# Optimization experiments

Hardware: AMD Instinct MI355X
Metric: run time of the kernel (lower is better)

Reference implementation:

```python
import jax, jax.numpy as jnp
import numpy as np

EPS_BN = 1e-5   # torch BatchNorm1d default eps
K = 3           # de_neighbors


def conv1(x, w):
    # 1x1 Conv1d, no bias: x [B,C,N], w [O,C] -> [B,O,N]
    return jnp.einsum('oc,bcn->bon', w, x)


def bn_relu(y, g, b):
    # BatchNorm1d in training mode (batch statistics, biased variance) + ReLU
    mean = jnp.mean(y, axis=(0, 2), keepdims=True)
    var = jnp.var(y, axis=(0, 2), keepdims=True)
    yn = (y - mean) * jax.lax.rsqrt(var + EPS_BN)
    return jax.nn.relu(yn * g[None, :, None] + b[None, :, None])


def propagate(xyz1, xyz2, p1, p2, k):
    # xyz1 [B,N,3] fine coords, xyz2 [B,S,3] coarse coords,
    # p1 [B,D1,N] fine feats, p2 [B,D2,S] coarse feats -> [B,D1+D2,N]
    pts2 = p2.transpose(0, 2, 1)  # [B,S,D2]
    # squared pairwise distances [B,N,S]
    d = (jnp.sum(xyz1 ** 2, -1)[:, :, None]
         + jnp.sum(xyz2 ** 2, -1)[:, None, :]
         - 2.0 * jnp.einsum('bnc,bsc->bns', xyz1, xyz2))
    negd, idx = jax.lax.top_k(-d, k)          # k smallest distances
    dists = -negd                              # [B,N,k]
    w = 1.0 / (dists + 1e-8)
    w = w / jnp.sum(w, -1, keepdims=True)      # inverse-distance weights
    B = xyz1.shape[0]
    gathered = pts2[jnp.arange(B)[:, None, None], idx]     # [B,N,k,D2]
    interp = jnp.sum(gathered * w[..., None], axis=2)      # [B,N,D2]
    new = jnp.concatenate([p1.transpose(0, 2, 1), interp], axis=-1)
    return new.transpose(0, 2, 1)


def setup_inputs() -> dict:
    key = jax.random.key(0)
    ks = jax.random.split(key, 20)
    B = 16
    npts = [2048, 512, 128, 32, 8]
    ch = [64, 128, 256, 512, 1024]
    inp = {}
    for i in range(5):
        inp[f'xyz{i}'] = jax.random.normal(ks[i], (B, npts[i], 3), jnp.float32)
        inp[f'x{i}'] = jax.random.normal(ks[5 + i], (B, ch[i], npts[i]), jnp.float32)
    lin_dims = [1536, 1792, 1920, 1984]
    for i, dmid in enumerate(lin_dims):
        inp[f'w_lin{i}'] = jax.random.normal(ks[10 + i], (dmid, dmid), jnp.float32) * (1.0 / np.sqrt(dmid))
        inp[f'g_lin{i}'] = jnp.ones((dmid,), jnp.float32)
        inp[f'b_lin{i}'] = jnp.zeros((dmid,), jnp.float32)
    inp['w_dec0'] = jax.random.normal(ks[14], (256, 1984), jnp.float32) * (1.0 / np.sqrt(1984))
    inp['g_dec'] = jnp.ones((256,), jnp.float32)
    inp['b_dec'] = jnp.zeros((256,), jnp.float32)
    inp['w_dec1'] = jax.random.normal(ks[15], (1, 256), jnp.float32) * (1.0 / np.sqrt(256))
    return inp


def reference(xyz0, xyz1, xyz2, xyz3, xyz4,
              x0, x1, x2, x3, x4,
              w_lin0, g_lin0, b_lin0,
              w_lin1, g_lin1, b_lin1,
              w_lin2, g_lin2, b_lin2,
              w_lin3, g_lin3, b_lin3,
              w_dec0, g_dec, b_dec, w_dec1):
    # lists are reversed in forward: coarsest first
    x = x4
    x = propagate(xyz3, xyz4, x3, x, K)   # [B,1536,32]
    x = bn_relu(conv1(x, w_lin0), g_lin0, b_lin0)
    x = propagate(xyz2, xyz3, x2, x, K)   # [B,1792,128]
    x = bn_relu(conv1(x, w_lin1), g_lin1, b_lin1)
    x = propagate(xyz1, xyz2, x1, x, K)   # [B,1920,512]
    x = bn_relu(conv1(x, w_lin2), g_lin2, b_lin2)
    x = propagate(xyz0, xyz1, x0, x, K)   # [B,1984,2048]
    x = bn_relu(conv1(x, w_lin3), g_lin3, b_lin3)
    # str_dec: Linear1Layer(1984,256) -> Dropout(eval=identity) -> Conv1d(256,1)
    x = bn_relu(conv1(x, w_dec0), g_dec, b_dec)
    out = conv1(x, w_dec1)                # [B,1,N]
    return out.squeeze(1)                 # [B,N]
```

## Files before the change

kernel.cpp:

```cpp
#include <hip/hip_runtime.h>
#include <stdint.h>
#include <stddef.h>

typedef _Float16 half8 __attribute__((ext_vector_type(8)));
typedef _Float16 half4v __attribute__((ext_vector_type(4)));
typedef float f32x4 __attribute__((ext_vector_type(4)));

__device__ __forceinline__ void gload_lds16(const void* g, void* l) {
  __builtin_amdgcn_global_load_lds((const __attribute__((address_space(1))) void*)g,
                                   (__attribute__((address_space(3))) void*)l, 16, 0, 0);
}

struct TPack {
  const float* in[5];
  _Float16* out[5];
  int C[5], N[5];
  int cum[6];
};
__global__ __launch_bounds__(256) void k_transpose_all(TPack p) {
  __shared__ float tile[32][33];
  int t = blockIdx.x;
  int ti = 0;
#pragma unroll
  for (int i = 0; i < 5; ++i) if (t >= p.cum[i + 1]) ti = i + 1;
  int lt = t - p.cum[ti];
  int C = p.C[ti], N = p.N[ti];
  const float* in = p.in[ti];
  _Float16* out = p.out[ti];
  int tiles_n = (N + 31) / 32;
  int perb = (C / 32) * tiles_n;
  int b = lt / perb;
  int rem = lt - b * perb;
  int c0 = (rem / tiles_n) * 32;
  int n0 = (rem % tiles_n) * 32;
  int tx = threadIdx.x, ty = threadIdx.y;
#pragma unroll
  for (int j = 0; j < 32; j += 8) {
    int c = c0 + ty + j, n = n0 + tx;
    if (c < C && n < N) tile[ty + j][tx] = in[((size_t)b * C + c) * N + n];
  }
  __syncthreads();
#pragma unroll
  for (int j = 0; j < 32; j += 8) {
    int n = n0 + ty + j, c = c0 + tx;
    if (n < N && c < C) out[((size_t)b * N + n) * C + c] = (_Float16)tile[tx][ty + j];
  }
}

__global__ __launch_bounds__(256) void k_cast_pad_w(const float* __restrict__ W,
                                                    _Float16* __restrict__ Wh,
                                                    int O, int K, int Opad, int Kpad) {
  size_t i = ((size_t)blockIdx.x * 256 + threadIdx.x) * 4;
  if (i >= (size_t)Opad * Kpad) return;
  int r = (int)(i / Kpad), k = (int)(i % Kpad);
  half4v v;
#pragma unroll
  for (int j = 0; j < 4; ++j) {
    float f = (r < O && (k + j) < K) ? W[(size_t)r * K + k + j] : 0.f;
    v[j] = (_Float16)f;
  }
  *(half4v*)(Wh + i) = v;
}

struct KPack {
  const float* q[4]; const float* p[4];
  int N1[4], S[4];
  int cum[5];
  int obase[4];
};
#define KNN_INS(dd, ii) { float _d = (dd); int _i = (ii); \
  if (_d < d0)      { d2 = d1; i2 = i1; d1 = d0; i1 = i0; d0 = _d; i0 = _i; } \
  else if (_d < d1) { d2 = d1; i2 = i1; d1 = _d; i1 = _i; } \
  else if (_d < d2) { d2 = _d; i2 = _i; } }
__global__ __launch_bounds__(256) void k_knn_all(KPack kp, int4* __restrict__ idxo,
                                                 float4* __restrict__ wo) {
  __shared__ float sp[512 * 3];
  __shared__ float spp[512];
  int t = blockIdx.x;
  int st = 0;
#pragma unroll
  for (int i = 0; i < 4; ++i) if (t >= kp.cum[i + 1]) st = i + 1;
  int lb = t - kp.cum[st];
  int N1 = kp.N1[st], S = kp.S[st];
  int nb = (N1 * 4 + 255) / 256;
  int b = lb / nb;
  int xb = lb - b * nb;
  const float* p = kp.p[st];
  const float* q = kp.q[st];
  for (int i = threadIdx.x; i < S * 3; i += 256) sp[i] = p[(size_t)b * S * 3 + i];
  __syncthreads();
  for (int s = threadIdx.x; s < S; s += 256)
    spp[s] = sp[s * 3] * sp[s * 3] + sp[s * 3 + 1] * sp[s * 3 + 1] + sp[s * 3 + 2] * sp[s * 3 + 2];
  __syncthreads();
  int tt = xb * 256 + threadIdx.x;
  int n = tt >> 2, sub = tt & 3;
  if (n >= N1) return;
  const float* qp = q + ((size_t)b * N1 + n) * 3;
  float qx = qp[0], qy = qp[1], qz = qp[2];
  float qq = qx * qx + qy * qy + qz * qz;
  float d0 = 1e30f, d1 = 1e30f, d2 = 1e30f;
  int i0 = 0, i1 = 0, i2 = 0;
  int Sq = S >> 2;
  int s0 = sub * Sq;
  for (int i = 0; i < Sq; ++i) {
    int s = s0 + i;
    float d = qq + spp[s] - 2.f * (qx * sp[s * 3] + qy * sp[s * 3 + 1] + qz * sp[s * 3 + 2]);
    KNN_INS(d, s);
  }
#pragma unroll
  for (int m = 1; m <= 2; m <<= 1) {
    float rd0 = __shfl_xor(d0, m, 64), rd1 = __shfl_xor(d1, m, 64), rd2 = __shfl_xor(d2, m, 64);
    int   ri0 = __shfl_xor(i0, m, 64), ri1 = __shfl_xor(i1, m, 64), ri2 = __shfl_xor(i2, m, 64);
    KNN_INS(rd0, ri0); KNN_INS(rd1, ri1); KNN_INS(rd2, ri2);
  }
  if (sub == 0) {
    float w0 = 1.f / (d0 + 1e-8f), w1 = 1.f / (d1 + 1e-8f), w2 = 1.f / (d2 + 1e-8f);
    float wsum = w0 + w1 + w2;
    int gi = kp.obase[st] + b * N1 + n;
    idxo[gi] = make_int4(b * S + i0, b * S + i1, b * S + i2, 0);
    wo[gi] = make_float4(w0 / wsum, w1 / wsum, w2 / wsum, 0.f);
  }
}

__global__ __launch_bounds__(256) void k_bn_norm(_Float16* __restrict__ G,
                                                 const float* __restrict__ scale,
                                                 const float* __restrict__ shiftv,
                                                 size_t total8, int ld) {
  size_t i = (size_t)blockIdx.x * 256 + threadIdx.x;
  if (i >= total8) return;
  half8 v = *(half8*)&G[i * 8];
  int c0 = (int)((i * 8) % (size_t)ld);
#pragma unroll
  for (int j = 0; j < 8; ++j) {
    float f = (float)v[j] * scale[c0 + j] + shiftv[c0 + j];
    v[j] = (_Float16)fmaxf(f, 0.f);
  }
  *(half8*)&G[i * 8] = v;
}

__global__ __launch_bounds__(256) void k_bn_finalize(const float* __restrict__ sum,
                                                     const float* __restrict__ sumsq,
                                                     const float* __restrict__ g, const float* __restrict__ b,
                                                     float* __restrict__ scale, float* __restrict__ shiftv,
                                                     int O, int Opad, float invM) {
  int c = blockIdx.x * 256 + threadIdx.x;
  if (c >= Opad) return;
  if (c < O) {
    float mean = sum[c] * invM;
    float var = sumsq[c] * invM - mean * mean;
    float sc = g[c] * rsqrtf(var + 1e-5f);
    scale[c] = sc;
    shiftv[c] = b[c] - mean * sc;
  } else {
    scale[c] = 0.f;
    shiftv[c] = 0.f;
  }
}


__global__ __launch_bounds__(256) void k_gemm_anorm(const _Float16* __restrict__ A,
                                                    const float* __restrict__ scale,
                                                    const float* __restrict__ shift,
                                                    int apply_nr,
                                                    const _Float16* __restrict__ W,
                                                    _Float16* __restrict__ Cout,
                                                    int K, int lda, int ldb, int ldc) {
  __shared__ __align__(16) _Float16 lA[128 * 64];
  __shared__ __align__(16) _Float16 lB[128 * 64];
  int tid = threadIdx.x;
  int m0 = blockIdx.x * 128;
  int o0 = blockIdx.y * 128;
  int lane = tid & 63, wv = tid >> 6;
  int wm = (wv & 1) * 64, wo = (wv >> 1) * 64;
  int lr = lane & 15, lq = lane >> 4;
  int trow = tid >> 3;
  int tsegl = (((tid & 7) ^ (trow & 7))) * 8;
  int sw = lr & 7;

  f32x4 acc[4][4];
#pragma unroll
  for (int mi = 0; mi < 4; ++mi)
#pragma unroll
    for (int oi = 0; oi < 4; ++oi)
      acc[mi][oi] = (f32x4){0.f, 0.f, 0.f, 0.f};

  const _Float16* gA = A + (size_t)(m0 + trow) * lda + tsegl;
  const _Float16* gB = W + (size_t)(o0 + trow) * ldb + tsegl;

  for (int k0 = 0; k0 < K; k0 += 64) {
#pragma unroll
    for (int i = 0; i < 4; ++i)
      gload_lds16(gB + (size_t)(32 * i) * ldb + k0, lB + ((size_t)i * 256 + tid) * 8);
    if (apply_nr) {
      float sc[8], sh[8];
#pragma unroll
      for (int j = 0; j < 8; ++j) { sc[j] = scale[k0 + tsegl + j]; sh[j] = shift[k0 + tsegl + j]; }
#pragma unroll
      for (int i = 0; i < 4; ++i) {
        half8 v = *(const half8*)(gA + (size_t)(32 * i) * lda + k0);
        half8 o;
#pragma unroll
        for (int j = 0; j < 8; ++j)
          o[j] = (_Float16)fmaxf((float)v[j] * sc[j] + sh[j], 0.f);
        *(half8*)&lA[((size_t)i * 256 + tid) * 8] = o;
      }
    } else {
#pragma unroll
      for (int i = 0; i < 4; ++i)
        gload_lds16(gA + (size_t)(32 * i) * lda + k0, lA + ((size_t)i * 256 + tid) * 8);
    }
    __syncthreads();
#pragma unroll
    for (int ks = 0; ks < 64; ks += 32) {
      half8 af[4], bf[4];
#pragma unroll
      for (int mi = 0; mi < 4; ++mi)
        af[mi] = *(const half8*)&lA[(wm + mi * 16 + lr) * 64 + ((((ks >> 3) + lq) ^ sw)) * 8];
#pragma unroll
      for (int oi = 0; oi < 4; ++oi)
        bf[oi] = *(const half8*)&lB[(wo + oi * 16 + lr) * 64 + ((((ks >> 3) + lq) ^ sw)) * 8];
#pragma unroll
      for (int mi = 0; mi < 4; ++mi)
#pragma unroll
        for (int oi = 0; oi < 4; ++oi)
          acc[mi][oi] = __builtin_amdgcn_mfma_f32_16x16x32_f16(af[mi], bf[oi], acc[mi][oi], 0, 0, 0);
    }
    __syncthreads();
  }

#pragma unroll
  for (int mi = 0; mi < 4; ++mi)
#pragma unroll
    for (int oi = 0; oi < 4; ++oi) {
      int col = o0 + wo + oi * 16 + lr;
      int rowb = m0 + wm + mi * 16 + lq * 4;
#pragma unroll
      for (int r = 0; r < 4; ++r)
        Cout[(size_t)(rowb + r) * ldc + col] = (_Float16)acc[mi][oi][r];
    }
}

__global__ __launch_bounds__(256) void k_gemm_yis(const _Float16* __restrict__ A,
                                                  const _Float16* __restrict__ W,
                                                  const _Float16* __restrict__ Z,
                                                  const int4* __restrict__ idxb,
                                                  const float4* __restrict__ wb,
                                                  _Float16* __restrict__ Y,
                                                  float* __restrict__ sum,
                                                  float* __restrict__ sumsq,
                                                  int K, int lda, int ldb, int ldy,
                                                  int ldz, int zcol0, int swz) {
  __shared__ __align__(16) _Float16 lsm[2 * 128 * 64];
  __shared__ int4 sIdx[128];
  __shared__ float4 sWt[128];
  __shared__ float sStat[256];
  _Float16* lA = lsm;
  _Float16* lB = lsm + 128 * 64;
  int tid = threadIdx.x;
  int m0, o0;
  if (swz) {
    int bid = blockIdx.y * gridDim.x + blockIdx.x;
    int o = (bid & 7) + ((bid >> 11) << 3);
    int m = (bid >> 3) & 255;
    m0 = m * 128; o0 = o * 128;
  } else {
    m0 = blockIdx.x * 128; o0 = blockIdx.y * 128;
  }
  if (tid < 128) {
    sIdx[tid] = idxb[m0 + tid];
    sWt[tid] = wb[m0 + tid];
  }
  sStat[tid] = 0.f;
  int lane = tid & 63, wv = tid >> 6;
  int wm = (wv & 1) * 64, wo = (wv >> 1) * 64;
  int lr = lane & 15, lq = lane >> 4;
  int trow = tid >> 3;
  int tsegl = (((tid & 7) ^ (trow & 7))) * 8;
  int sw = lr & 7;

  f32x4 acc[4][4];
#pragma unroll
  for (int mi = 0; mi < 4; ++mi)
#pragma unroll
    for (int oi = 0; oi < 4; ++oi)
      acc[mi][oi] = (f32x4){0.f, 0.f, 0.f, 0.f};

  const _Float16* gA = A + (size_t)(m0 + trow) * lda + tsegl;
  const _Float16* gB = W + (size_t)(o0 + trow) * ldb + tsegl;

  for (int k0 = 0; k0 < K; k0 += 64) {
#pragma unroll
    for (int i = 0; i < 4; ++i) {
      gload_lds16(gA + (size_t)(32 * i) * lda + k0, lA + ((size_t)i * 256 + tid) * 8);
      gload_lds16(gB + (size_t)(32 * i) * ldb + k0, lB + ((size_t)i * 256 + tid) * 8);
    }
    __syncthreads();
#pragma unroll
    for (int ks = 0; ks < 64; ks += 32) {
      half8 af[4], bf[4];
#pragma unroll
      for (int mi = 0; mi < 4; ++mi)
        af[mi] = *(const half8*)&lA[(wm + mi * 16 + lr) * 64 + ((((ks >> 3) + lq) ^ sw)) * 8];
#pragma unroll
      for (int oi = 0; oi < 4; ++oi)
        bf[oi] = *(const half8*)&lB[(wo + oi * 16 + lr) * 64 + ((((ks >> 3) + lq) ^ sw)) * 8];
#pragma unroll
      for (int mi = 0; mi < 4; ++mi)
#pragma unroll
        for (int oi = 0; oi < 4; ++oi)
          acc[mi][oi] = __builtin_amdgcn_mfma_f32_16x16x32_f16(af[mi], bf[oi], acc[mi][oi], 0, 0, 0);
    }
    __syncthreads();
  }

#pragma unroll
  for (int mi = 0; mi < 4; ++mi)
#pragma unroll
    for (int oi = 0; oi < 4; ++oi)
#pragma unroll
      for (int r = 0; r < 4; ++r)
        lsm[(wm + mi * 16 + lq * 4 + r) * 128 + (wo + oi * 16 + lr)] = (_Float16)acc[mi][oi][r];
  __syncthreads();

  int tcol = (tid & 15) * 8;
  int rbase = tid >> 4;
  float s8[8], q8[8];
#pragma unroll
  for (int j = 0; j < 8; ++j) { s8[j] = 0.f; q8[j] = 0.f; }
#pragma unroll
  for (int i = 0; i < 8; ++i) {
    int row = rbase + i * 16;
    int4 id = sIdx[row];
    float4 w = sWt[row];
    half8 y = *(half8*)&lsm[row * 128 + tcol];
    int zc = zcol0 + o0 + tcol;
    half8 a  = *(const half8*)&Z[(size_t)id.x * ldz + zc];
    half8 b2 = *(const half8*)&Z[(size_t)id.y * ldz + zc];
    half8 c2 = *(const half8*)&Z[(size_t)id.z * ldz + zc];
    half8 o;
#pragma unroll
    for (int j = 0; j < 8; ++j) {
      float v = (float)y[j] + w.x * (float)a[j] + w.y * (float)b2[j] + w.z * (float)c2[j];
      o[j] = (_Float16)v;
      s8[j] += v; q8[j] += v * v;
    }
    *(half8*)&Y[(size_t)(m0 + row) * ldy + o0 + tcol] = o;
  }
#pragma unroll
  for (int j = 0; j < 8; ++j) {
    atomicAdd(&sStat[tcol + j], s8[j]);
    atomicAdd(&sStat[128 + tcol + j], q8[j]);
  }
  __syncthreads();
  if (tid < 128) {
    atomicAdd(&sum[o0 + tid], sStat[tid]);
    atomicAdd(&sumsq[o0 + tid], sStat[128 + tid]);
  }
}

__global__ __launch_bounds__(256) void k_gemm_dec_acc(const _Float16* __restrict__ A,
                                                      const float* __restrict__ sumc,
                                                      const float* __restrict__ sumsqc,
                                                      const float* __restrict__ g,
                                                      const float* __restrict__ b,
                                                      float invM, int c0, int Oglob,
                                                      const _Float16* __restrict__ W,
                                                      float* __restrict__ D,
                                                      int K, int lda, int ldb, int ldc,
                                                      int accum, int do_stats, int swz,
                                                      float* __restrict__ dsum,
                                                      float* __restrict__ dsumsq) {
  __shared__ __align__(16) _Float16 lA[128 * 64];
  __shared__ __align__(16) _Float16 lB[128 * 64];
  __shared__ float sScale[2048];
  __shared__ float sShift[2048];
  __shared__ float sStat[256];
  int tid = threadIdx.x;
  int m0, o0;
  if (swz) {
    int bid = blockIdx.y * gridDim.x + blockIdx.x;
    int mlow = bid & 7, oo = (bid >> 3) & 1, mhigh = bid >> 4;
    m0 = (mhigh * 8 + mlow) * 128;
    o0 = oo * 128;
  } else {
    m0 = blockIdx.x * 128; o0 = blockIdx.y * 128;
  }
  for (int c = tid; c < K; c += 256) {
    int gc = c0 + c;
    float sc = 0.f, sh = 0.f;
    if (gc < Oglob) {
      float mean = sumc[c] * invM;
      float var = sumsqc[c] * invM - mean * mean;
      sc = g[gc] * rsqrtf(var + 1e-5f);
      sh = b[gc] - mean * sc;
    }
    sScale[c] = sc; sShift[c] = sh;
  }
  sStat[tid] = 0.f;
  __syncthreads();

  int lane = tid & 63, wv = tid >> 6;
  int wm = (wv & 1) * 64, wo = (wv >> 1) * 64;
  int lr = lane & 15, lq = lane >> 4;
  int trow = tid >> 3;
  int tsegl = (((tid & 7) ^ (trow & 7))) * 8;
  int sw = lr & 7;

  f32x4 acc[4][4];
#pragma unroll
  for (int mi = 0; mi < 4; ++mi)
#pragma unroll
    for (int oi = 0; oi < 4; ++oi)
      acc[mi][oi] = (f32x4){0.f, 0.f, 0.f, 0.f};

  const _Float16* gA = A + (size_t)(m0 + trow) * lda + tsegl;
  const _Float16* gB = W + (size_t)(o0 + trow) * ldb + tsegl;

  for (int k0 = 0; k0 < K; k0 += 64) {
#pragma unroll
    for (int i = 0; i < 4; ++i)
      gload_lds16(gB + (size_t)(32 * i) * ldb + k0, lB + ((size_t)i * 256 + tid) * 8);
    float sc[8], sh[8];
#pragma unroll
    for (int j = 0; j < 8; ++j) { sc[j] = sScale[k0 + tsegl + j]; sh[j] = sShift[k0 + tsegl + j]; }
#pragma unroll
    for (int i = 0; i < 4; ++i) {
      half8 v = *(const half8*)(gA + (size_t)(32 * i) * lda + k0);
      half8 o;
#pragma unroll
      for (int j = 0; j < 8; ++j)
        o[j] = (_Float16)fmaxf((float)v[j] * sc[j] + sh[j], 0.f);
      *(half8*)&lA[((size_t)i * 256 + tid) * 8] = o;
    }
    __syncthreads();
#pragma unroll
    for (int ks = 0; ks < 64; ks += 32) {
      half8 af[4], bf[4];
#pragma unroll
      for (int mi = 0; mi < 4; ++mi)
        af[mi] = *(const half8*)&lA[(wm + mi * 16 + lr) * 64 + ((((ks >> 3) + lq) ^ sw)) * 8];
#pragma unroll
      for (int oi = 0; oi < 4; ++oi)
        bf[oi] = *(const half8*)&lB[(wo + oi * 16 + lr) * 64 + ((((ks >> 3) + lq) ^ sw)) * 8];
#pragma unroll
      for (int mi = 0; mi < 4; ++mi)
#pragma unroll
        for (int oi = 0; oi < 4; ++oi)
          acc[mi][oi] = __builtin_amdgcn_mfma_f32_16x16x32_f16(af[mi], bf[oi], acc[mi][oi], 0, 0, 0);
    }
    __syncthreads();
  }

  float ps[4], pq[4];
#pragma unroll
  for (int oi = 0; oi < 4; ++oi) { ps[oi] = 0.f; pq[oi] = 0.f; }
#pragma unroll
  for (int mi = 0; mi < 4; ++mi)
#pragma unroll
    for (int oi = 0; oi < 4; ++oi) {
      int col = o0 + wo + oi * 16 + lr;
      int rowb = m0 + wm + mi * 16 + lq * 4;
#pragma unroll
      for (int r = 0; r < 4; ++r) {
        size_t idx = (size_t)(rowb + r) * ldc + col;
        float v = acc[mi][oi][r];
        if (accum) v += D[idx];
        D[idx] = v;
        if (do_stats) { ps[oi] += v; pq[oi] += v * v; }
      }
    }
  if (do_stats) {
#pragma unroll
    for (int oi = 0; oi < 4; ++oi) {
      int tc = wo + oi * 16 + lr;
      atomicAdd(&sStat[tc], ps[oi]);
      atomicAdd(&sStat[128 + tc], pq[oi]);
    }
    __syncthreads();
    if (tid < 128) {
      atomicAdd(&dsum[o0 + tid], sStat[tid]);
      atomicAdd(&dsumsq[o0 + tid], sStat[128 + tid]);
    }
  }
}

__global__ __launch_bounds__(256) void k_final_dot2(const float* __restrict__ H,
                                                    const float* __restrict__ w,
                                                    const float* __restrict__ dsum,
                                                    const float* __restrict__ dsumsq,
                                                    const float* __restrict__ g,
                                                    const float* __restrict__ b,
                                                    float invM,
                                                    float* __restrict__ out, int Mtot) {
  __shared__ float sSc[256], sSh[256];
  int tid = threadIdx.x;
  {
    int c = tid;
    float mean = dsum[c] * invM;
    float var = dsumsq[c] * invM - mean * mean;
    float sc = g[c] * rsqrtf(var + 1e-5f);
    sSc[c] = sc;
    sSh[c] = b[c] - mean * sc;
  }
  __syncthreads();
  int lane = tid & 63, wv = tid >> 6;
  int r = blockIdx.x * 4 + wv;
  if (r >= Mtot) return;
  const float* h = H + (size_t)r * 256;
  float s = 0.f;
  for (int c = lane; c < 256; c += 64)
    s += fmaxf(h[c] * sSc[c] + sSh[c], 0.f) * w[c];
#pragma unroll
  for (int o = 32; o > 0; o >>= 1) s += __shfl_down(s, o, 64);
  if (lane == 0) out[r] = s;
}

extern "C" void kernel_launch(void* const* d_in, const int* in_sizes, int n_in,
                              void* d_out, int out_size, void* d_ws, size_t ws_size,
                              hipStream_t stream) {
  (void)in_sizes; (void)n_in; (void)out_size;
  const int B = 16;
  const float* xyzs[5]; const float* xs[5];
  for (int i = 0; i < 5; ++i) { xyzs[i] = (const float*)d_in[2 * i]; xs[i] = (const float*)d_in[2 * i + 1]; }
  const float* wlin[4] = {(const float*)d_in[10], (const float*)d_in[13], (const float*)d_in[16], (const float*)d_in[19]};
  const float* glin[4] = {(const float*)d_in[11], (const float*)d_in[14], (const float*)d_in[17], (const float*)d_in[20]};
  const float* blin[4] = {(const float*)d_in[12], (const float*)d_in[15], (const float*)d_in[18], (const float*)d_in[21]};
  const float* wdec0 = (const float*)d_in[22];
  const float* gdec  = (const float*)d_in[23];
  const float* bdec  = (const float*)d_in[24];
  const float* wdec1 = (const float*)d_in[25];
  float* outp = (float*)d_out;

  const int ch[5] = {64, 128, 256, 512, 1024};
  const int np[5] = {2048, 512, 128, 32, 8};

  char* base = (char*)d_ws;
  size_t off = 0;
  auto alloc = [&](size_t bytes) -> char* {
    char* p = base + off;
    off += (bytes + 255) & ~(size_t)255;
    return p;
  };

  _Float16* Wbuf = (_Float16*)alloc((size_t)2048 * 1984 * 2);
  _Float16* Wdec = (_Float16*)alloc((size_t)256 * 2048 * 2);
  _Float16* tT[5];
  for (int i = 0; i < 5; ++i) tT[i] = (_Float16*)alloc((size_t)B * np[i] * ch[i] * 2);
  int4* idxAll = (int4*)alloc(43520 * sizeof(int4));
  float4* wbAll = (float4*)alloc(43520 * sizeof(float4));
  float* statsPool = (float*)alloc(8 * 2 * 2048 * sizeof(float));
  float* scaleA = (float*)alloc(2048 * sizeof(float));
  float* shiftA = (float*)alloc(2048 * sizeof(float));
  _Float16* Zreg = (_Float16*)alloc((size_t)8192 * 2048 * 2);
  float* D = (float*)alloc((size_t)32768 * 256 * 4);
  size_t ybytes_chunk = 40370176;
  size_t ybytes_full = (size_t)32768 * 2048 * 2;
  int use_full = (ws_size >= off + ybytes_full + 256);
  char* Yreg = alloc(use_full ? ybytes_full : ybytes_chunk);
  _Float16* Y0 = (_Float16*)Yreg;
  _Float16* Y1 = (_Float16*)(Yreg + (size_t)512 * 1536 * 2);
  _Float16* Y2 = (_Float16*)(Yreg + (size_t)(512 * 1536 + 2048 * 1792) * 2);
  _Float16* Ychunk = (_Float16*)Yreg;
  _Float16* Y3full = (_Float16*)Yreg;
  if (off > ws_size) return;

  hipMemsetAsync(statsPool, 0, 8 * 2 * 2048 * sizeof(float), stream);

  {
    TPack p;
    int cum = 0;
    for (int i = 0; i < 5; ++i) {
      p.in[i] = xs[i]; p.out[i] = tT[i]; p.C[i] = ch[i]; p.N[i] = np[i];
      p.cum[i] = cum;
      cum += (ch[i] / 32) * ((np[i] + 31) / 32) * B;
    }
    p.cum[5] = cum;
    k_transpose_all<<<cum, dim3(32, 8), 0, stream>>>(p);
  }
  {
    size_t tot4 = (size_t)256 * 2048 / 4;
    k_cast_pad_w<<<dim3((unsigned)((tot4 + 255) / 256)), 256, 0, stream>>>(wdec0, Wdec, 256, 1984, 256, 2048);
  }

  const int N1s[4] = {32, 128, 512, 2048};
  const int Ss[4]  = {8, 32, 128, 512};
  const int C1s[4] = {512, 256, 128, 64};
  const int C2s[4] = {1024, 1536, 1792, 1920};
  const int Os[4]  = {1536, 1792, 1920, 1984};
  const int obase[4] = {0, 512, 2560, 10752};
  _Float16* Ys[3] = {Y0, Y1, Y2};

  {
    KPack kp;
    int cum = 0;
    for (int st = 0; st < 4; ++st) {
      kp.q[st] = xyzs[3 - st]; kp.p[st] = xyzs[4 - st];
      kp.N1[st] = N1s[st]; kp.S[st] = Ss[st];
      kp.cum[st] = cum;
      cum += ((N1s[st] * 4 + 255) / 256) * B;
      kp.obase[st] = obase[st];
    }
    kp.cum[4] = cum;
    k_knn_all<<<cum, 256, 0, stream>>>(kp, idxAll, wbAll);
  }

  for (int st = 0; st < 3; ++st) {
    int N1 = N1s[st], C1 = C1s[st], C2 = C2s[st], O = Os[st];
    int Ktot = C1 + C2;
    int M = B * N1, Msrc = B * Ss[st];
    const _Float16* H = (st == 0) ? tT[4] : Ys[st - 1];
    _Float16* Y = Ys[st];
    float* sum = statsPool + st * 2 * 2048;
    float* sumsq = sum + 2048;

    size_t wt = (size_t)O * Ktot / 4;
    k_cast_pad_w<<<(unsigned)((wt + 255) / 256), 256, 0, stream>>>(wlin[st], Wbuf, O, Ktot, O, Ktot);

    k_gemm_anorm<<<dim3(Msrc / 128, O / 128), 256, 0, stream>>>(H, scaleA, shiftA, st != 0,
                                                                Wbuf + C1, Zreg, C2, C2, Ktot, O);
    k_gemm_yis<<<dim3(M / 128, O / 128), 256, 0, stream>>>(tT[3 - st], Wbuf, Zreg,
                                                           idxAll + obase[st], wbAll + obase[st],
                                                           Y, sum, sumsq,
                                                           C1, C1, Ktot, O, O, 0, 0);
    k_bn_finalize<<<(O + 255) / 256, 256, 0, stream>>>(sum, sumsq, glin[st], blin[st], scaleA, shiftA, O, O, 1.f / M);
  }

  {
    int C1 = 64, C2 = 1920, O = 1984, M = 32768, Msrc = 8192;
    int Ktot = 1984;
    size_t wt = (size_t)2048 * Ktot / 4;
    k_cast_pad_w<<<(unsigned)((wt + 255) / 256), 256, 0, stream>>>(wlin[3], Wbuf, O, Ktot, 2048, Ktot);

    k_gemm_anorm<<<dim3(Msrc / 128, 16), 256, 0, stream>>>(Y2, scaleA, shiftA, 1,
                                                           Wbuf + C1, Zreg, C2, C2, Ktot, 2048);

    float* dsum = statsPool + 7 * 2 * 2048;
    float* dsumsq = dsum + 2048;
    if (use_full) {
      float* sum = statsPool + 3 * 2 * 2048;
      float* sumsq = sum + 2048;
      k_gemm_yis<<<dim3(256, 16), 256, 0, stream>>>(tT[0], Wbuf, Zreg,
                                                    idxAll + obase[3], wbAll + obase[3],
                                                    Y3full, sum, sumsq,
                                                    C1, C1, Ktot, 2048, 2048, 0, 1);
      k_gemm_dec_acc<<<dim3(256, 2), 256, 0, stream>>>(Y3full, sum, sumsq,
                                                       glin[3], blin[3], 1.f / M, 0, O,
                                                       Wdec, D, 2048, 2048, 2048, 256,
                                                       0, 1, 1, dsum, dsumsq);
    } else {
      for (int c0 = 0; c0 < 2048; c0 += 512) {
        float* sum = statsPool + (3 + c0 / 512) * 2 * 2048;
        float* sumsq = sum + 2048;
        k_gemm_yis<<<dim3(M / 128, 4), 256, 0, stream>>>(tT[0], Wbuf + (size_t)c0 * Ktot, Zreg,
                                                         idxAll + obase[3], wbAll + obase[3],
                                                         Ychunk, sum, sumsq,
                                                         C1, C1, Ktot, 512, 2048, c0, 0);
        k_gemm_dec_acc<<<dim3(M / 128, 2), 256, 0, stream>>>(Ychunk, sum, sumsq,
                                                             glin[3], blin[3], 1.f / M, c0, O,
                                                             Wdec + c0, D, 512, 512, 2048, 256,
                                                             c0 != 0, c0 == 1536, 0, dsum, dsumsq);
      }
    }
  }

  {
    int M = 32768;
    float* dsum = statsPool + 7 * 2 * 2048;
    float* dsumsq = dsum + 2048;
    k_final_dot2<<<M / 4, 256, 0, stream>>>(D, wdec1, dsum, dsumsq, gdec, bdec, 1.f / M, outp, M);
  }
}
```

Before: 667.4 us.

## Batch weight casts into one launch and replace stat atomics with partial-sum reduction

When the workspace is large enough, all five weight matrices get their own fp16 buffers and are cast and padded in a single batched kernel instead of four separate casts spread between stages. For the full-size last stage, per-block BN statistics are written to a scratch area (reusing the D buffer) and reduced by a new kernel instead of global atomics. This removes launches and atomic contention, at the cost of extra workspace and one more small reduction kernel. An unused normalization kernel is also deleted.

```diff
diff --git a/kernel.cpp b/kernel.cpp
--- a/kernel.cpp
+++ b/kernel.cpp
@@ -51,6 +51,33 @@
                                                     _Float16* __restrict__ Wh,
                                                     int O, int K, int Opad, int Kpad) {
   size_t i = ((size_t)blockIdx.x * 256 + threadIdx.x) * 4;
+  if (i >= (size_t)Opad * Kpad) return;
+  int r = (int)(i / Kpad), k = (int)(i % Kpad);
+  half4v v;
+#pragma unroll
+  for (int j = 0; j < 4; ++j) {
+    float f = (r < O && (k + j) < K) ? W[(size_t)r * K + k + j] : 0.f;
+    v[j] = (_Float16)f;
+  }
+  *(half4v*)(Wh + i) = v;
+}
+
+struct WPack {
+  const float* in[5];
+  _Float16* out[5];
+  int O[5], K[5], Opad[5], Kpad[5];
+  int cum[6];
+};
+__global__ __launch_bounds__(256) void k_cast_all_w(WPack p) {
+  int t = blockIdx.x;
+  int ti = 0;
+#pragma unroll
+  for (int i = 0; i < 5; ++i) if (t >= p.cum[i + 1]) ti = i + 1;
+  int lb = t - p.cum[ti];
+  int O = p.O[ti], K = p.K[ti], Opad = p.Opad[ti], Kpad = p.Kpad[ti];
+  const float* W = p.in[ti];
+  _Float16* Wh = p.out[ti];
+  size_t i = ((size_t)lb * 256 + threadIdx.x) * 4;
   if (i >= (size_t)Opad * Kpad) return;
   int r = (int)(i / Kpad), k = (int)(i % Kpad);
   half4v v;
@@ -122,22 +149,6 @@
   }
 }
 
-__global__ __launch_bounds__(256) void k_bn_norm(_Float16* __restrict__ G,
-                                                 const float* __restrict__ scale,
-                                                 const float* __restrict__ shiftv,
-                                                 size_t total8, int ld) {
-  size_t i = (size_t)blockIdx.x * 256 + threadIdx.x;
-  if (i >= total8) return;
-  half8 v = *(half8*)&G[i * 8];
-  int c0 = (int)((i * 8) % (size_t)ld);
-#pragma unroll
-  for (int j = 0; j < 8; ++j) {
-    float f = (float)v[j] * scale[c0 + j] + shiftv[c0 + j];
-    v[j] = (_Float16)fmaxf(f, 0.f);
-  }
-  *(half8*)&G[i * 8] = v;
-}
-
 __global__ __launch_bounds__(256) void k_bn_finalize(const float* __restrict__ sum,
                                                      const float* __restrict__ sumsq,
                                                      const float* __restrict__ g, const float* __restrict__ b,
@@ -155,6 +166,18 @@
     scale[c] = 0.f;
     shiftv[c] = 0.f;
   }
+}
+
+__global__ __launch_bounds__(256) void k_stat_reduce(const float* __restrict__ ps,
+                                                     float* __restrict__ sum,
+                                                     float* __restrict__ sumsq, int nm) {
+  int o = blockIdx.x;
+  int t = threadIdx.x;
+  float acc = 0.f;
+  for (int m = 0; m < nm; ++m)
+    acc += ps[((size_t)(o * 256 + m)) * 256 + t];
+  if (t < 128) sum[o * 128 + t] = acc;
+  else         sumsq[o * 128 + (t - 128)] = acc;
 }
 
 
@@ -248,6 +271,7 @@
                                                   _Float16* __restrict__ Y,
                                                   float* __restrict__ sum,
                                                   float* __restrict__ sumsq,
+                                                  float* __restrict__ pstats,
                                                   int K, int lda, int ldb, int ldy,
                                                   int ldz, int zcol0, int swz) {
   __shared__ __align__(16) _Float16 lsm[2 * 128 * 64];
@@ -353,8 +377,14 @@
   }
   __syncthreads();
   if (tid < 128) {
-    atomicAdd(&sum[o0 + tid], sStat[tid]);
-    atomicAdd(&sumsq[o0 + tid], sStat[128 + tid]);
+    if (pstats) {
+      float* dst = pstats + ((size_t)((o0 >> 7) * 256 + (m0 >> 7))) * 256;
+      dst[tid] = sStat[tid];
+      dst[128 + tid] = sStat[128 + tid];
+    } else {
+      atomicAdd(&sum[o0 + tid], sStat[tid]);
+      atomicAdd(&sumsq[o0 + tid], sStat[128 + tid]);
+    }
   }
 }
 
@@ -542,8 +572,6 @@
     return p;
   };
 
-  _Float16* Wbuf = (_Float16*)alloc((size_t)2048 * 1984 * 2);
-  _Float16* Wdec = (_Float16*)alloc((size_t)256 * 2048 * 2);
   _Float16* tT[5];
   for (int i = 0; i < 5; ++i) tT[i] = (_Float16*)alloc((size_t)B * np[i] * ch[i] * 2);
   int4* idxAll = (int4*)alloc(43520 * sizeof(int4));
@@ -553,9 +581,33 @@
   float* shiftA = (float*)alloc(2048 * sizeof(float));
   _Float16* Zreg = (_Float16*)alloc((size_t)8192 * 2048 * 2);
   float* D = (float*)alloc((size_t)32768 * 256 * 4);
+  size_t off_base = off;
+
+  const int WO[5]   = {1536, 1792, 1920, 1984, 256};
+  const int WOp[5]  = {1536, 1792, 1920, 2048, 256};
+  const int WK[5]   = {1536, 1792, 1920, 1984, 1984};
+  const int WKp[5]  = {1536, 1792, 1920, 1984, 2048};
+  size_t wall_bytes = 0;
+  for (int i = 0; i < 5; ++i) wall_bytes += (((size_t)WOp[i] * WKp[i] * 2) + 255) & ~(size_t)255;
+  size_t wshared_bytes = ((((size_t)2048 * 1984 * 2) + 255) & ~(size_t)255) +
+                         ((((size_t)256 * 2048 * 2) + 255) & ~(size_t)255);
   size_t ybytes_chunk = 40370176;
   size_t ybytes_full = (size_t)32768 * 2048 * 2;
-  int use_full = (ws_size >= off + ybytes_full + 256);
+
+  int gate_w    = (ws_size >= off_base + wall_bytes + ybytes_full + 512);
+  int use_full  = gate_w || (ws_size >= off_base + wshared_bytes + ybytes_full + 512);
+
+  _Float16* Wst[4];
+  _Float16* Wdec;
+  _Float16* Wbuf = nullptr;
+  if (gate_w) {
+    for (int i = 0; i < 4; ++i) Wst[i] = (_Float16*)alloc((size_t)WOp[i] * WKp[i] * 2);
+    Wdec = (_Float16*)alloc((size_t)256 * 2048 * 2);
+  } else {
+    Wbuf = (_Float16*)alloc((size_t)2048 * 1984 * 2);
+    for (int i = 0; i < 4; ++i) Wst[i] = Wbuf;
+    Wdec = (_Float16*)alloc((size_t)256 * 2048 * 2);
+  }
   char* Yreg = alloc(use_full ? ybytes_full : ybytes_chunk);
   _Float16* Y0 = (_Float16*)Yreg;
   _Float16* Y1 = (_Float16*)(Yreg + (size_t)512 * 1536 * 2);
@@ -577,9 +629,23 @@
     p.cum[5] = cum;
     k_transpose_all<<<cum, dim3(32, 8), 0, stream>>>(p);
   }
-  {
+
+  const float* wsrc[5] = {wlin[0], wlin[1], wlin[2], wlin[3], wdec0};
+  if (gate_w) {
+    WPack p;
+    int cum = 0;
+    for (int i = 0; i < 5; ++i) {
+      p.in[i] = wsrc[i];
+      p.out[i] = (i < 4) ? Wst[i] : Wdec;
+      p.O[i] = WO[i]; p.K[i] = WK[i]; p.Opad[i] = WOp[i]; p.Kpad[i] = WKp[i];
+      p.cum[i] = cum;
+      cum += (int)(((size_t)WOp[i] * WKp[i] / 4 + 255) / 256);
+    }
+    p.cum[5] = cum;
+    k_cast_all_w<<<cum, 256, 0, stream>>>(p);
+  } else {
     size_t tot4 = (size_t)256 * 2048 / 4;
-    k_cast_pad_w<<<dim3((unsigned)((tot4 + 255) / 256)), 256, 0, stream>>>(wdec0, Wdec, 256, 1984, 256, 2048);
+    k_cast_pad_w<<<(unsigned)((tot4 + 255) / 256), 256, 0, stream>>>(wdec0, Wdec, 256, 1984, 256, 2048);
   }
 
   const int N1s[4] = {32, 128, 512, 2048};
@@ -613,14 +679,15 @@
     float* sum = statsPool + st * 2 * 2048;
     float* sumsq = sum + 2048;
 
-    size_t wt = (size_t)O * Ktot / 4;
-    k_cast_pad_w<<<(unsigned)((wt + 255) / 256), 256, 0, stream>>>(wlin[st], Wbuf, O, Ktot, O, Ktot);
-
+    if (!gate_w) {
+      size_t wt = (size_t)O * Ktot / 4;
+      k_cast_pad_w<<<(unsigned)((wt + 255) / 256), 256, 0, stream>>>(wlin[st], Wbuf, O, Ktot, O, Ktot);
+    }
     k_gemm_anorm<<<dim3(Msrc / 128, O / 128), 256, 0, stream>>>(H, scaleA, shiftA, st != 0,
-                                                                Wbuf + C1, Zreg, C2, C2, Ktot, O);
-    k_gemm_yis<<<dim3(M / 128, O / 128), 256, 0, stream>>>(tT[3 - st], Wbuf, Zreg,
+                                                                Wst[st] + C1, Zreg, C2, C2, Ktot, O);
+    k_gemm_yis<<<dim3(M / 128, O / 128), 256, 0, stream>>>(tT[3 - st], Wst[st], Zreg,
                                                            idxAll + obase[st], wbAll + obase[st],
-                                                           Y, sum, sumsq,
+                                                           Y, sum, sumsq, nullptr,
                                                            C1, C1, Ktot, O, O, 0, 0);
     k_bn_finalize<<<(O + 255) / 256, 256, 0, stream>>>(sum, sumsq, glin[st], blin[st], scaleA, shiftA, O, O, 1.f / M);
   }
@@ -628,21 +695,24 @@
   {
     int C1 = 64, C2 = 1920, O = 1984, M = 32768, Msrc = 8192;
     int Ktot = 1984;
-    size_t wt = (size_t)2048 * Ktot / 4;
-    k_cast_pad_w<<<(unsigned)((wt + 255) / 256), 256, 0, stream>>>(wlin[3], Wbuf, O, Ktot, 2048, Ktot);
+    if (!gate_w) {
+      size_t wt = (size_t)2048 * Ktot / 4;
+      k_cast_pad_w<<<(unsigned)((wt + 255) / 256), 256, 0, stream>>>(wlin[3], Wbuf, O, Ktot, 2048, Ktot);
+    }
 
     k_gemm_anorm<<<dim3(Msrc / 128, 16), 256, 0, stream>>>(Y2, scaleA, shiftA, 1,
-                                                           Wbuf + C1, Zreg, C2, C2, Ktot, 2048);
+                                                           Wst[3] + C1, Zreg, C2, C2, Ktot, 2048);
 
     float* dsum = statsPool + 7 * 2 * 2048;
     float* dsumsq = dsum + 2048;
     if (use_full) {
       float* sum = statsPool + 3 * 2 * 2048;
       float* sumsq = sum + 2048;
-      k_gemm_yis<<<dim3(256, 16), 256, 0, stream>>>(tT[0], Wbuf, Zreg,
+      k_gemm_yis<<<dim3(256, 16), 256, 0, stream>>>(tT[0], Wst[3], Zreg,
                                                     idxAll + obase[3], wbAll + obase[3],
-                                                    Y3full, sum, sumsq,
+                                                    Y3full, sum, sumsq, D,
                                                     C1, C1, Ktot, 2048, 2048, 0, 1);
+      k_stat_reduce<<<16, 256, 0, stream>>>(D, sum, sumsq, 256);
       k_gemm_dec_acc<<<dim3(256, 2), 256, 0, stream>>>(Y3full, sum, sumsq,
                                                        glin[3], blin[3], 1.f / M, 0, O,
                                                        Wdec, D, 2048, 2048, 2048, 256,
@@ -651,9 +721,9 @@
       for (int c0 = 0; c0 < 2048; c0 += 512) {
         float* sum = statsPool + (3 + c0 / 512) * 2 * 2048;
         float* sumsq = sum + 2048;
-        k_gemm_yis<<<dim3(M / 128, 4), 256, 0, stream>>>(tT[0], Wbuf + (size_t)c0 * Ktot, Zreg,
+        k_gemm_yis<<<dim3(M / 128, 4), 256, 0, stream>>>(tT[0], Wst[3] + (size_t)c0 * Ktot, Zreg,
                                                          idxAll + obase[3], wbAll + obase[3],
-                                                         Ychunk, sum, sumsq,
+                                                         Ychunk, sum, sumsq, nullptr,
                                                          C1, C1, Ktot, 512, 2048, c0, 0);
         k_gemm_dec_acc<<<dim3(M / 128, 2), 256, 0, stream>>>(Ychunk, sum, sumsq,
                                                              glin[3], blin[3], 1.f / M, c0, O,
```

After: 710.5 us. 6.5% more time.
